# Kernel tuning notes

Hardware: AMD Instinct MI355X
Metric: run time of the kernel (lower is better)

Reference implementation:

```python
import jax, jax.numpy as jnp
import numpy as np

D_MODEL = 1024
N_HEADS = 16
D_HIDDEN = 4096
EPS = 1e-6
SCALE = float(np.sqrt(D_MODEL // N_HEADS))


def setup_inputs() -> dict:
    key = jax.random.key(0)
    ks = jax.random.split(key, 12)
    d, h = D_MODEL, D_HIDDEN
    init = lambda k, shape, fan_in: jax.random.uniform(k, shape, jnp.float32, -1.0, 1.0) / np.sqrt(fan_in)
    return {
        "x": jax.random.normal(ks[0], (2, 2048, d), jnp.float32),
        "W_q": init(ks[1], (d, d), d),
        "W_k": init(ks[2], (d, d), d),
        "W_v": init(ks[3], (d, d), d),
        "W_o": init(ks[4], (d, d), d),
        "b_o": init(ks[5], (d,), d),
        "attn_norm_w": 1.0 + jax.random.normal(ks[6], (d,), jnp.float32) / np.sqrt(d),
        "ffn_norm_w": 1.0 + jax.random.normal(ks[7], (d,), jnp.float32) / np.sqrt(d),
        "W_gate": init(ks[8], (d, h), d),
        "W_hidden": init(ks[9], (d, h), d),
        "W_out": init(ks[10], (h, d), h),
        "b_out": init(ks[11], (d,), h),
    }


def rmsnorm(x, w):
    return w * x * jax.lax.rsqrt(jnp.mean(x * x, axis=-1, keepdims=True) + EPS)


def attention(x, W_q, W_k, W_v, W_o, b_o):
    b, l, d = x.shape
    hd = d // N_HEADS
    split = lambda t: t.reshape(b, l, N_HEADS, hd).transpose(0, 2, 1, 3)  # b n l d
    q = split(x @ W_q)
    k = split(x @ W_k)
    v = split(x @ W_v)
    scores = jnp.einsum('bnld,bnmd->bnlm', q, k) / SCALE
    attn = jax.nn.softmax(scores, axis=-1)
    out = jnp.einsum('bnlm,bnmd->bnld', attn, v)
    out = out.transpose(0, 2, 1, 3).reshape(b, l, d)
    return out @ W_o + b_o


def swiglu(x, W_gate, W_hidden, W_out, b_out):
    return (jax.nn.silu(x @ W_gate) * (x @ W_hidden)) @ W_out + b_out


def reference(x, W_q, W_k, W_v, W_o, b_o, attn_norm_w, ffn_norm_w, W_gate, W_hidden, W_out, b_out):
    x = x + attention(rmsnorm(x, attn_norm_w), W_q, W_k, W_v, W_o, b_o)
    return x + swiglu(rmsnorm(x, ffn_norm_w), W_gate, W_hidden, W_out, b_out)
```

## Files before the change

kernel.cpp:

```cpp
#include <hip/hip_runtime.h>
#include <stdint.h>
#include <stddef.h>

typedef unsigned short ushort_t;
typedef __attribute__((ext_vector_type(8))) unsigned short us8;
typedef __attribute__((ext_vector_type(4))) unsigned short us4;
typedef __attribute__((ext_vector_type(2))) unsigned int u32x2;
typedef __attribute__((ext_vector_type(8))) short bf16x8;
typedef __attribute__((ext_vector_type(4))) float f32x4;
typedef __attribute__((ext_vector_type(4))) float f4;

#define DM 1024
#define SEQ 2048
#define NBATCH 2
#define NHEADS 16
#define HDIM 64
#define DH 4096
#define ROWS 4096

__device__ __forceinline__ float bf2f(ushort_t u) {
  union { unsigned int i; float f; } v; v.i = ((unsigned int)u) << 16; return v.f;
}
__device__ __forceinline__ ushort_t f2bf(float f) {
  union { float f; unsigned int i; } v; v.f = f;
  unsigned int x = v.i;
  unsigned int r = (x + 0x7FFFu + ((x >> 16) & 1u)) >> 16;
  return (ushort_t)r;
}

__global__ void transpose_f32_bf16(const float* __restrict__ in,
                                   ushort_t* __restrict__ out, int R, int C) {
  __shared__ ushort_t tile[64][68];
  int t = threadIdx.x;
  int c0 = blockIdx.x * 64, r0 = blockIdx.y * 64;
#pragma unroll
  for (int i = 0; i < 4; ++i) {
    int c = i * 256 + t;
    int row = c >> 4;
    int col4 = (c & 15) * 4;
    f4 v = *(const f4*)(in + (size_t)(r0 + row) * C + c0 + col4);
#pragma unroll
    for (int j = 0; j < 4; ++j) tile[row][col4 + j] = f2bf(v[j]);
  }
  __syncthreads();
#pragma unroll
  for (int i = 0; i < 4; ++i) {
    int c = i * 256 + t;
    int orow = c >> 4;
    int col4 = (c & 15) * 4;
    us4 v;
#pragma unroll
    for (int j = 0; j < 4; ++j) v[j] = tile[col4 + j][orow];
    *(us4*)(out + (size_t)(c0 + orow) * R + r0 + col4) = v;
  }
}

__global__ void rmsnorm_kernel(const float* __restrict__ x,
                               const float* __restrict__ w,
                               ushort_t* __restrict__ y) {
  int row = blockIdx.x;
  int t = threadIdx.x;
  f4 xv = *(const f4*)(x + (size_t)row * DM + t * 4);
  float s = 0.f;
#pragma unroll
  for (int j = 0; j < 4; ++j) s += xv[j] * xv[j];
#pragma unroll
  for (int off = 32; off >= 1; off >>= 1) s += __shfl_xor(s, off);
  __shared__ float wsum[4];
  if ((t & 63) == 0) wsum[t >> 6] = s;
  __syncthreads();
  float tot = wsum[0] + wsum[1] + wsum[2] + wsum[3];
  float scale = rsqrtf(tot * (1.0f / DM) + 1e-6f);
  f4 wv = *(const f4*)(w + t * 4);
  us4 o;
#pragma unroll
  for (int j = 0; j < 4; ++j) o[j] = f2bf(xv[j] * wv[j] * scale);
  *(us4*)(y + (size_t)row * DM + t * 4) = o;
}

template <int EPI>
__global__ __launch_bounds__(256) void gemm_bt(
    const ushort_t* __restrict__ A, const ushort_t* __restrict__ Bt,
    void* __restrict__ Cv, int M, int N, int K,
    const float* __restrict__ bias, const void* __restrict__ resv) {
  __shared__ __align__(16) ushort_t As[128 * 64];
  __shared__ __align__(16) ushort_t Bs[128 * 64];
  int tid = threadIdx.x;
  int l = tid & 63, w = tid >> 6;
  int wm = w >> 1, wn = w & 1;
  int m0 = blockIdx.y * 128, n0 = blockIdx.x * 128;
  int lr = l & 15, lk = (l >> 4) * 8;
  f32x4 acc[4][4] = {};
  const ushort_t* Ag = A + (size_t)m0 * K;
  const ushort_t* Bg = Bt + (size_t)n0 * K;
  int srow = tid >> 3;
  int scol = (tid & 7) * 8;

  for (int kt = 0; kt < K; kt += 64) {
#pragma unroll
    for (int i = 0; i < 4; ++i) {
      int r2 = i * 32 + srow;
      int c = i * 256 + tid;
      __builtin_amdgcn_global_load_lds(
          (const __attribute__((address_space(1))) unsigned int*)(Ag + (size_t)r2 * K + kt + scol),
          (__attribute__((address_space(3))) unsigned int*)(&As[c * 8]), 16, 0, 0);
      __builtin_amdgcn_global_load_lds(
          (const __attribute__((address_space(1))) unsigned int*)(Bg + (size_t)r2 * K + kt + scol),
          (__attribute__((address_space(3))) unsigned int*)(&Bs[c * 8]), 16, 0, 0);
    }
    __syncthreads();
#pragma unroll
    for (int kk = 0; kk < 2; ++kk) {
      bf16x8 a[4], b[4];
#pragma unroll
      for (int i = 0; i < 4; ++i) {
        a[i] = *(const bf16x8*)(&As[(wm * 64 + i * 16 + lr) * 64 + kk * 32 + lk]);
        b[i] = *(const bf16x8*)(&Bs[(wn * 64 + i * 16 + lr) * 64 + kk * 32 + lk]);
      }
#pragma unroll
      for (int i = 0; i < 4; ++i)
#pragma unroll
        for (int j = 0; j < 4; ++j)
          acc[i][j] = __builtin_amdgcn_mfma_f32_16x16x32_bf16(a[i], b[j], acc[i][j], 0, 0, 0);
    }
    __syncthreads();
  }

  int r0 = (l >> 4) * 4;
#pragma unroll
  for (int i = 0; i < 4; ++i) {
#pragma unroll
    for (int r = 0; r < 4; ++r) {
      int grow = m0 + wm * 64 + i * 16 + r0 + r;
#pragma unroll
      for (int j = 0; j < 4; ++j) {
        int gcol = n0 + wn * 64 + j * 16 + lr;
        size_t idx = (size_t)grow * N + gcol;
        float v = acc[i][j][r];
        if (EPI == 0) {
          ((ushort_t*)Cv)[idx] = f2bf(v);
        } else if (EPI == 1) {
          float r2 = ((const float*)resv)[idx];
          ((float*)Cv)[idx] = v + bias[gcol] + r2;
        } else {
          float g = bf2f(((const ushort_t*)resv)[idx]);
          ((ushort_t*)Cv)[idx] = f2bf(v * g / (1.0f + __expf(-g)));
        }
      }
    }
  }
}

#define LDP 72

__global__ __launch_bounds__(256) void attn_mfma(
    const ushort_t* __restrict__ Qp, const ushort_t* __restrict__ Kp,
    const ushort_t* __restrict__ Vp, ushort_t* __restrict__ Op,
    int qs, int os) {
  __shared__ __align__(16) ushort_t Qs[64 * LDP];
  __shared__ __align__(16) ushort_t Ks[64 * LDP];
  __shared__ __align__(16) ushort_t Vs[64 * LDP];
  __shared__ __align__(16) ushort_t Ps[4][16 * LDP];
  int tid = threadIdx.x;
  int l = tid & 63;
  int w = tid >> 6;
  int g = l >> 4;
  int q = l & 15;
  int h = blockIdx.y, b = blockIdx.z;
  int q0 = blockIdx.x * 64;
  const size_t base = (size_t)b * SEQ * qs + h * HDIM;
  const size_t obase = (size_t)b * SEQ * os + h * HDIM;

#pragma unroll
  for (int i = 0; i < 2; ++i) {
    int cc = i * 256 + tid;
    int row = cc >> 3, d8 = (cc & 7) * 8;
    *(us8*)(&Qs[row * LDP + d8]) =
        *(const us8*)(Qp + base + (size_t)(q0 + row) * qs + d8);
  }

  float m_run = -3.0e38f, l_run = 0.f;
  f32x4 oacc[4] = {};

  for (int kv = 0; kv < SEQ; kv += 64) {
    __syncthreads();
#pragma unroll
    for (int i = 0; i < 2; ++i) {
      int cc = i * 256 + tid;
      int row = cc >> 3, d8 = (cc & 7) * 8;
      *(us8*)(&Ks[row * LDP + d8]) =
          *(const us8*)(Kp + base + (size_t)(kv + row) * qs + d8);
      us8 vv = *(const us8*)(Vp + base + (size_t)(kv + row) * qs + d8);
      int m8 = (d8 >> 3) & 7;
      int keysw = row ^ (m8 << 3);
#pragma unroll
      for (int j = 0; j < 8; ++j)
        Vs[(d8 + j) * LDP + keysw] = vv[j];
    }
    __syncthreads();

    f32x4 sacc[4] = {};
#pragma unroll
    for (int kk = 0; kk < 2; ++kk) {
      bf16x8 qf = *(const bf16x8*)(&Qs[(w * 16 + q) * LDP + kk * 32 + g * 8]);
#pragma unroll
      for (int t = 0; t < 4; ++t) {
        bf16x8 kf = *(const bf16x8*)(&Ks[(t * 16 + q) * LDP + kk * 32 + g * 8]);
        sacc[t] = __builtin_amdgcn_mfma_f32_16x16x32_bf16(kf, qf, sacc[t], 0, 0, 0);
      }
    }

    float mt = -3.0e38f;
#pragma unroll
    for (int t = 0; t < 4; ++t)
#pragma unroll
      for (int r = 0; r < 4; ++r) mt = fmaxf(mt, sacc[t][r]);
    mt = fmaxf(mt, __shfl_xor(mt, 16));
    mt = fmaxf(mt, __shfl_xor(mt, 32));
    mt *= 0.125f;
    float m_new = fmaxf(m_run, mt);
    float alpha = __expf(m_run - m_new);
    float psum = 0.f;
#pragma unroll
    for (int t = 0; t < 4; ++t) {
      float p0 = __expf(fmaf(sacc[t][0], 0.125f, -m_new));
      float p1 = __expf(fmaf(sacc[t][1], 0.125f, -m_new));
      float p2 = __expf(fmaf(sacc[t][2], 0.125f, -m_new));
      float p3 = __expf(fmaf(sacc[t][3], 0.125f, -m_new));
      psum += (p0 + p1) + (p2 + p3);
      u32x2 d;
      d[0] = (unsigned int)f2bf(p0) | ((unsigned int)f2bf(p1) << 16);
      d[1] = (unsigned int)f2bf(p2) | ((unsigned int)f2bf(p3) << 16);
      *(u32x2*)(&Ps[w][q * LDP + t * 16 + g * 4]) = d;
    }
    m_run = m_new;
    l_run = l_run * alpha + psum;
#pragma unroll
    for (int t = 0; t < 4; ++t)
#pragma unroll
      for (int r = 0; r < 4; ++r) oacc[t][r] *= alpha;

    __asm__ volatile("s_waitcnt lgkmcnt(0)" ::: "memory");

#pragma unroll
    for (int kk = 0; kk < 2; ++kk) {
      bf16x8 pf = *(const bf16x8*)(&Ps[w][q * LDP + kk * 32 + g * 8]);
#pragma unroll
      for (int t = 0; t < 4; ++t) {
        int d = t * 16 + q;
        int keyoff = (kk * 32 + g * 8) ^ (((d >> 3) & 7) << 3);
        bf16x8 vf = *(const bf16x8*)(&Vs[d * LDP + keyoff]);
        oacc[t] = __builtin_amdgcn_mfma_f32_16x16x32_bf16(vf, pf, oacc[t], 0, 0, 0);
      }
    }
  }

  l_run += __shfl_xor(l_run, 16);
  l_run += __shfl_xor(l_run, 32);
  float inv = 1.f / l_run;
#pragma unroll
  for (int t = 0; t < 4; ++t) {
    us4 o;
#pragma unroll
    for (int r = 0; r < 4; ++r) o[r] = f2bf(oacc[t][r] * inv);
    *(us4*)(Op + obase + (size_t)(q0 + w * 16 + q) * os + t * 16 + g * 4) = o;
  }
}

extern "C" void kernel_launch(void* const* d_in, const int* in_sizes, int n_in,
                              void* d_out, int out_size, void* d_ws, size_t ws_size,
                              hipStream_t stream) {
  const float* x   = (const float*)d_in[0];
  const float* Wq  = (const float*)d_in[1];
  const float* Wk  = (const float*)d_in[2];
  const float* Wv  = (const float*)d_in[3];
  const float* Wo  = (const float*)d_in[4];
  const float* bo  = (const float*)d_in[5];
  const float* anw = (const float*)d_in[6];
  const float* fnw = (const float*)d_in[7];
  const float* Wg  = (const float*)d_in[8];
  const float* Wh  = (const float*)d_in[9];
  const float* Wu  = (const float*)d_in[10];
  const float* bu  = (const float*)d_in[11];

  char* wsb = (char*)d_ws;
  ushort_t* WqkvT = (ushort_t*)(wsb + 0);
  ushort_t* WoT   = (ushort_t*)(wsb + (6u << 20));
  ushort_t* WgT   = (ushort_t*)(wsb + (8u << 20));
  ushort_t* WhT   = (ushort_t*)(wsb + (16u << 20));
  ushort_t* WuT   = (ushort_t*)(wsb + (24u << 20));
  ushort_t* hb    = (ushort_t*)(wsb + (32u << 20));
  ushort_t* qkvb  = (ushort_t*)(wsb + (40u << 20));
  ushort_t* ab    = (ushort_t*)(wsb + (64u << 20));
  ushort_t* gb    = (ushort_t*)(wsb + (40u << 20));
  float* out = (float*)d_out;

  transpose_f32_bf16<<<dim3(16, 16), 256, 0, stream>>>(Wq, WqkvT, DM, DM);
  transpose_f32_bf16<<<dim3(16, 16), 256, 0, stream>>>(Wk, WqkvT + DM * DM, DM, DM);
  transpose_f32_bf16<<<dim3(16, 16), 256, 0, stream>>>(Wv, WqkvT + 2 * DM * DM, DM, DM);
  transpose_f32_bf16<<<dim3(16, 16), 256, 0, stream>>>(Wo, WoT, DM, DM);
  transpose_f32_bf16<<<dim3(64, 16), 256, 0, stream>>>(Wg, WgT, DM, DH);
  transpose_f32_bf16<<<dim3(64, 16), 256, 0, stream>>>(Wh, WhT, DM, DH);
  transpose_f32_bf16<<<dim3(16, 64), 256, 0, stream>>>(Wu, WuT, DH, DM);

  rmsnorm_kernel<<<ROWS, 256, 0, stream>>>(x, anw, hb);
  gemm_bt<0><<<dim3(24, 32), 256, 0, stream>>>(hb, WqkvT, qkvb, ROWS, 3 * DM, DM, nullptr, nullptr);
  attn_mfma<<<dim3(SEQ / 64, NHEADS, NBATCH), 256, 0, stream>>>(
      qkvb, qkvb + DM, qkvb + 2 * DM, ab, 3 * DM, DM);
  gemm_bt<1><<<dim3(8, 32), 256, 0, stream>>>(ab, WoT, out, ROWS, DM, DM, bo, x);

  rmsnorm_kernel<<<ROWS, 256, 0, stream>>>(out, fnw, hb);
  gemm_bt<0><<<dim3(32, 32), 256, 0, stream>>>(hb, WgT, gb, ROWS, DH, DM, nullptr, nullptr);
  gemm_bt<2><<<dim3(32, 32), 256, 0, stream>>>(hb, WhT, gb, ROWS, DH, DM, nullptr, gb);
  gemm_bt<1><<<dim3(8, 32), 256, 0, stream>>>(gb, WuT, out, ROWS, DM, DH, bu, out);
}
```

Baseline: 509.1 us.

## Pre-transpose V, batch weight transposes, and use 64-row tiles for narrow GEMMs

Merges the seven weight transpose launches into one kernel indexed by blockIdx.y. Adds a kernel that writes V transposed per head into scratch space in the output buffer, so attention loads V with contiguous vector stores instead of scattered per-element LDS writes. Templates the GEMM on M tile size and uses 64-row tiles for the N=1024 projections to double the block count on a 256-CU device. The costs are an extra pass over V and lower data reuse per block in the narrow GEMMs.

```diff
diff --git a/kernel.cpp b/kernel.cpp
--- a/kernel.cpp
+++ b/kernel.cpp
@@ -28,17 +28,35 @@
   return (ushort_t)r;
 }
 
-__global__ void transpose_f32_bf16(const float* __restrict__ in,
-                                   ushort_t* __restrict__ out, int R, int C) {
+__global__ void transpose_all(const float* __restrict__ Wq, const float* __restrict__ Wk,
+                              const float* __restrict__ Wv, const float* __restrict__ Wo,
+                              const float* __restrict__ Wg, const float* __restrict__ Wh,
+                              const float* __restrict__ Wu,
+                              ushort_t* __restrict__ WqkvT, ushort_t* __restrict__ WoT,
+                              ushort_t* __restrict__ WgT, ushort_t* __restrict__ WhT,
+                              ushort_t* __restrict__ WuT) {
+  const float* src; ushort_t* dst; int R, C;
+  switch (blockIdx.y) {
+    case 0: src = Wq; dst = WqkvT;                R = DM; C = DM; break;
+    case 1: src = Wk; dst = WqkvT + DM * DM;      R = DM; C = DM; break;
+    case 2: src = Wv; dst = WqkvT + 2 * DM * DM;  R = DM; C = DM; break;
+    case 3: src = Wo; dst = WoT;                  R = DM; C = DM; break;
+    case 4: src = Wg; dst = WgT;                  R = DM; C = DH; break;
+    case 5: src = Wh; dst = WhT;                  R = DM; C = DH; break;
+    default: src = Wu; dst = WuT;                 R = DH; C = DM; break;
+  }
+  int nbx = C >> 6, nby = R >> 6;
+  int bid = blockIdx.x;
+  if (bid >= nbx * nby) return;
+  int c0 = (bid % nbx) * 64, r0 = (bid / nbx) * 64;
+
   __shared__ ushort_t tile[64][68];
   int t = threadIdx.x;
-  int c0 = blockIdx.x * 64, r0 = blockIdx.y * 64;
 #pragma unroll
   for (int i = 0; i < 4; ++i) {
     int c = i * 256 + t;
-    int row = c >> 4;
-    int col4 = (c & 15) * 4;
-    f4 v = *(const f4*)(in + (size_t)(r0 + row) * C + c0 + col4);
+    int row = c >> 4, col4 = (c & 15) * 4;
+    f4 v = *(const f4*)(src + (size_t)(r0 + row) * C + c0 + col4);
 #pragma unroll
     for (int j = 0; j < 4; ++j) tile[row][col4 + j] = f2bf(v[j]);
   }
@@ -46,12 +64,11 @@
 #pragma unroll
   for (int i = 0; i < 4; ++i) {
     int c = i * 256 + t;
-    int orow = c >> 4;
-    int col4 = (c & 15) * 4;
+    int orow = c >> 4, col4 = (c & 15) * 4;
     us4 v;
 #pragma unroll
     for (int j = 0; j < 4; ++j) v[j] = tile[col4 + j][orow];
-    *(us4*)(out + (size_t)(c0 + orow) * R + r0 + col4) = v;
+    *(us4*)(dst + (size_t)(c0 + orow) * R + r0 + col4) = v;
   }
 }
 
@@ -78,19 +95,20 @@
   *(us4*)(y + (size_t)row * DM + t * 4) = o;
 }
 
-template <int EPI>
+template <int EPI, int TM>
 __global__ __launch_bounds__(256) void gemm_bt(
     const ushort_t* __restrict__ A, const ushort_t* __restrict__ Bt,
     void* __restrict__ Cv, int M, int N, int K,
     const float* __restrict__ bias, const void* __restrict__ resv) {
-  __shared__ __align__(16) ushort_t As[128 * 64];
+  constexpr int FI = TM / 32;
+  __shared__ __align__(16) ushort_t As[TM * 64];
   __shared__ __align__(16) ushort_t Bs[128 * 64];
   int tid = threadIdx.x;
   int l = tid & 63, w = tid >> 6;
   int wm = w >> 1, wn = w & 1;
-  int m0 = blockIdx.y * 128, n0 = blockIdx.x * 128;
+  int m0 = blockIdx.y * TM, n0 = blockIdx.x * 128;
   int lr = l & 15, lk = (l >> 4) * 8;
-  f32x4 acc[4][4] = {};
+  f32x4 acc[FI][4] = {};
   const ushort_t* Ag = A + (size_t)m0 * K;
   const ushort_t* Bg = Bt + (size_t)n0 * K;
   int srow = tid >> 3;
@@ -98,27 +116,29 @@
 
   for (int kt = 0; kt < K; kt += 64) {
 #pragma unroll
+    for (int i = 0; i < TM / 32; ++i) {
+      __builtin_amdgcn_global_load_lds(
+          (const __attribute__((address_space(1))) unsigned int*)(Ag + (size_t)(i * 32 + srow) * K + kt + scol),
+          (__attribute__((address_space(3))) unsigned int*)(&As[(i * 256 + tid) * 8]), 16, 0, 0);
+    }
+#pragma unroll
     for (int i = 0; i < 4; ++i) {
-      int r2 = i * 32 + srow;
-      int c = i * 256 + tid;
       __builtin_amdgcn_global_load_lds(
-          (const __attribute__((address_space(1))) unsigned int*)(Ag + (size_t)r2 * K + kt + scol),
-          (__attribute__((address_space(3))) unsigned int*)(&As[c * 8]), 16, 0, 0);
-      __builtin_amdgcn_global_load_lds(
-          (const __attribute__((address_space(1))) unsigned int*)(Bg + (size_t)r2 * K + kt + scol),
-          (__attribute__((address_space(3))) unsigned int*)(&Bs[c * 8]), 16, 0, 0);
+          (const __attribute__((address_space(1))) unsigned int*)(Bg + (size_t)(i * 32 + srow) * K + kt + scol),
+          (__attribute__((address_space(3))) unsigned int*)(&Bs[(i * 256 + tid) * 8]), 16, 0, 0);
     }
     __syncthreads();
 #pragma unroll
     for (int kk = 0; kk < 2; ++kk) {
-      bf16x8 a[4], b[4];
-#pragma unroll
-      for (int i = 0; i < 4; ++i) {
-        a[i] = *(const bf16x8*)(&As[(wm * 64 + i * 16 + lr) * 64 + kk * 32 + lk]);
-        b[i] = *(const bf16x8*)(&Bs[(wn * 64 + i * 16 + lr) * 64 + kk * 32 + lk]);
-      }
-#pragma unroll
-      for (int i = 0; i < 4; ++i)
+      bf16x8 a[FI], b[4];
+#pragma unroll
+      for (int i = 0; i < FI; ++i)
+        a[i] = *(const bf16x8*)(&As[(wm * (TM / 2) + i * 16 + lr) * 64 + kk * 32 + lk]);
+#pragma unroll
+      for (int j = 0; j < 4; ++j)
+        b[j] = *(const bf16x8*)(&Bs[(wn * 64 + j * 16 + lr) * 64 + kk * 32 + lk]);
+#pragma unroll
+      for (int i = 0; i < FI; ++i)
 #pragma unroll
         for (int j = 0; j < 4; ++j)
           acc[i][j] = __builtin_amdgcn_mfma_f32_16x16x32_bf16(a[i], b[j], acc[i][j], 0, 0, 0);
@@ -128,10 +148,10 @@
 
   int r0 = (l >> 4) * 4;
 #pragma unroll
-  for (int i = 0; i < 4; ++i) {
+  for (int i = 0; i < FI; ++i) {
 #pragma unroll
     for (int r = 0; r < 4; ++r) {
-      int grow = m0 + wm * 64 + i * 16 + r0 + r;
+      int grow = m0 + wm * (TM / 2) + i * 16 + r0 + r;
 #pragma unroll
       for (int j = 0; j < 4; ++j) {
         int gcol = n0 + wn * 64 + j * 16 + lr;
@@ -151,11 +171,37 @@
   }
 }
 
+__global__ void vtrans_kernel(const ushort_t* __restrict__ qkv,
+                              ushort_t* __restrict__ VT) {
+  __shared__ ushort_t tile[64][72];
+  int t = threadIdx.x;
+  int s0 = blockIdx.x * 64;
+  int h = blockIdx.y, b = blockIdx.z;
+  const ushort_t* src = qkv + (size_t)b * SEQ * (3 * DM) + 2 * DM + h * HDIM;
+  ushort_t* dst = VT + ((size_t)(b * NHEADS + h) * HDIM) * SEQ;
+#pragma unroll
+  for (int i = 0; i < 2; ++i) {
+    int c = i * 256 + t;
+    int srow = c >> 3, d8 = (c & 7) * 8;
+    *(us8*)(&tile[srow][d8]) = *(const us8*)(src + (size_t)(s0 + srow) * (3 * DM) + d8);
+  }
+  __syncthreads();
+#pragma unroll
+  for (int i = 0; i < 2; ++i) {
+    int c = i * 256 + t;
+    int drow = c >> 3, s8 = (c & 7) * 8;
+    us8 v;
+#pragma unroll
+    for (int j = 0; j < 8; ++j) v[j] = tile[s8 + j][drow];
+    *(us8*)(dst + (size_t)drow * SEQ + s0 + s8) = v;
+  }
+}
+
 #define LDP 72
 
 __global__ __launch_bounds__(256) void attn_mfma(
     const ushort_t* __restrict__ Qp, const ushort_t* __restrict__ Kp,
-    const ushort_t* __restrict__ Vp, ushort_t* __restrict__ Op,
+    const ushort_t* __restrict__ VT, ushort_t* __restrict__ Op,
     int qs, int os) {
   __shared__ __align__(16) ushort_t Qs[64 * LDP];
   __shared__ __align__(16) ushort_t Ks[64 * LDP];
@@ -170,6 +216,7 @@
   int q0 = blockIdx.x * 64;
   const size_t base = (size_t)b * SEQ * qs + h * HDIM;
   const size_t obase = (size_t)b * SEQ * os + h * HDIM;
+  const ushort_t* Vb = VT + ((size_t)(b * NHEADS + h) * HDIM) * SEQ;
 
 #pragma unroll
   for (int i = 0; i < 2; ++i) {
@@ -190,12 +237,8 @@
       int row = cc >> 3, d8 = (cc & 7) * 8;
       *(us8*)(&Ks[row * LDP + d8]) =
           *(const us8*)(Kp + base + (size_t)(kv + row) * qs + d8);
-      us8 vv = *(const us8*)(Vp + base + (size_t)(kv + row) * qs + d8);
-      int m8 = (d8 >> 3) & 7;
-      int keysw = row ^ (m8 << 3);
-#pragma unroll
-      for (int j = 0; j < 8; ++j)
-        Vs[(d8 + j) * LDP + keysw] = vv[j];
+      *(us8*)(&Vs[row * LDP + d8]) =
+          *(const us8*)(Vb + (size_t)row * SEQ + kv + d8);
     }
     __syncthreads();
 
@@ -247,9 +290,7 @@
       bf16x8 pf = *(const bf16x8*)(&Ps[w][q * LDP + kk * 32 + g * 8]);
 #pragma unroll
       for (int t = 0; t < 4; ++t) {
-        int d = t * 16 + q;
-        int keyoff = (kk * 32 + g * 8) ^ (((d >> 3) & 7) << 3);
-        bf16x8 vf = *(const bf16x8*)(&Vs[d * LDP + keyoff]);
+        bf16x8 vf = *(const bf16x8*)(&Vs[(t * 16 + q) * LDP + kk * 32 + g * 8]);
         oacc[t] = __builtin_amdgcn_mfma_f32_16x16x32_bf16(vf, pf, oacc[t], 0, 0, 0);
       }
     }
@@ -293,24 +334,21 @@
   ushort_t* qkvb  = (ushort_t*)(wsb + (40u << 20));
   ushort_t* ab    = (ushort_t*)(wsb + (64u << 20));
   ushort_t* gb    = (ushort_t*)(wsb + (40u << 20));
+  ushort_t* VT    = (ushort_t*)d_out;
   float* out = (float*)d_out;
 
-  transpose_f32_bf16<<<dim3(16, 16), 256, 0, stream>>>(Wq, WqkvT, DM, DM);
-  transpose_f32_bf16<<<dim3(16, 16), 256, 0, stream>>>(Wk, WqkvT + DM * DM, DM, DM);
-  transpose_f32_bf16<<<dim3(16, 16), 256, 0, stream>>>(Wv, WqkvT + 2 * DM * DM, DM, DM);
-  transpose_f32_bf16<<<dim3(16, 16), 256, 0, stream>>>(Wo, WoT, DM, DM);
-  transpose_f32_bf16<<<dim3(64, 16), 256, 0, stream>>>(Wg, WgT, DM, DH);
-  transpose_f32_bf16<<<dim3(64, 16), 256, 0, stream>>>(Wh, WhT, DM, DH);
-  transpose_f32_bf16<<<dim3(16, 64), 256, 0, stream>>>(Wu, WuT, DH, DM);
+  transpose_all<<<dim3(1024, 7), 256, 0, stream>>>(Wq, Wk, Wv, Wo, Wg, Wh, Wu,
+                                                   WqkvT, WoT, WgT, WhT, WuT);
 
   rmsnorm_kernel<<<ROWS, 256, 0, stream>>>(x, anw, hb);
-  gemm_bt<0><<<dim3(24, 32), 256, 0, stream>>>(hb, WqkvT, qkvb, ROWS, 3 * DM, DM, nullptr, nullptr);
+  gemm_bt<0, 128><<<dim3(24, 32), 256, 0, stream>>>(hb, WqkvT, qkvb, ROWS, 3 * DM, DM, nullptr, nullptr);
+  vtrans_kernel<<<dim3(SEQ / 64, NHEADS, NBATCH), 256, 0, stream>>>(qkvb, VT);
   attn_mfma<<<dim3(SEQ / 64, NHEADS, NBATCH), 256, 0, stream>>>(
-      qkvb, qkvb + DM, qkvb + 2 * DM, ab, 3 * DM, DM);
-  gemm_bt<1><<<dim3(8, 32), 256, 0, stream>>>(ab, WoT, out, ROWS, DM, DM, bo, x);
+      qkvb, qkvb + DM, VT, ab, 3 * DM, DM);
+  gemm_bt<1, 64><<<dim3(8, 64), 256, 0, stream>>>(ab, WoT, out, ROWS, DM, DM, bo, x);
 
   rmsnorm_kernel<<<ROWS, 256, 0, stream>>>(out, fnw, hb);
-  gemm_bt<0><<<dim3(32, 32), 256, 0, stream>>>(hb, WgT, gb, ROWS, DH, DM, nullptr, nullptr);
-  gemm_bt<2><<<dim3(32, 32), 256, 0, stream>>>(hb, WhT, gb, ROWS, DH, DM, nullptr, gb);
-  gemm_bt<1><<<dim3(8, 32), 256, 0, stream>>>(gb, WuT, out, ROWS, DM, DH, bu, out);
-}
+  gemm_bt<0, 128><<<dim3(32, 32), 256, 0, stream>>>(hb, WgT, gb, ROWS, DH, DM, nullptr, nullptr);
+  gemm_bt<2, 128><<<dim3(32, 32), 256, 0, stream>>>(hb, WhT, gb, ROWS, DH, DM, nullptr, gb);
+  gemm_bt<1, 64><<<dim3(8, 64), 256, 0, stream>>>(gb, WuT, out, ROWS, DM, DH, bu, out);
+}
```

After: 482.4 us. 1.06x faster.
